# Kernel optimization log

Measured on AMD Instinct MI355X. Metric: run time of the kernel, lower is better.

## Reference

```python
import jax, jax.numpy as jnp
import numpy as np

B, T, F = 512, 512, 16
UNITS = [64, 32, 32, 32]
VOCAB, EDIM = 1281, 4


def setup_inputs() -> dict:
    key = jax.random.key(0)
    ks = jax.random.split(key, 32)
    x = jax.random.normal(ks[0], (B, T, F), jnp.float32)
    # column 1 holds integer org ids (stored as float, as in the TF model)
    ids = jax.random.randint(ks[1], (B, T), 0, VOCAB).astype(jnp.float32)
    x = x.at[:, :, 1].set(ids)
    d = {"input_tensor": x,
         "emb": jax.random.normal(ks[2], (VOCAB, EDIM), jnp.float32) * 0.05}
    din = 1 + (F - 2) + EDIM  # 18
    i = 3
    for l, u in enumerate(UNITS):
        d[f"k{l}"] = jax.random.normal(ks[i], (din, 3 * u), jnp.float32) * 0.1; i += 1
        d[f"r{l}"] = jax.random.normal(ks[i], (u, 3 * u), jnp.float32) * 0.1; i += 1
        d[f"bi{l}"] = jnp.zeros((3 * u,), jnp.float32)
        d[f"bh{l}"] = jnp.zeros((3 * u,), jnp.float32)
        din = u
    u = UNITS[-1]
    d["w1"] = jax.random.normal(ks[i], (u, u), jnp.float32) * 0.1; i += 1
    d["b1"] = jnp.zeros((u,), jnp.float32)
    d["w2"] = jax.random.normal(ks[i], (u, u), jnp.float32) * 0.1; i += 1
    d["b2"] = jnp.zeros((u,), jnp.float32)
    d["v"] = jax.random.normal(ks[i], (u, 1), jnp.float32) * 0.1; i += 1
    d["bv"] = jnp.zeros((1,), jnp.float32)
    d["wd"] = jax.random.normal(ks[i], (u, 2), jnp.float32) * 0.1; i += 1
    d["bd"] = jnp.zeros((2,), jnp.float32)
    return d


def _gru(h, xp, rk, bh):
    # Keras GRUCell (reset_after=True). xp = x @ kernel + input_bias, [B, 3u]
    hp = h @ rk + bh
    xz, xr, xh = jnp.split(xp, 3, axis=-1)
    hz, hr, hhp = jnp.split(hp, 3, axis=-1)
    z = jax.nn.sigmoid(xz + hz)
    r = jax.nn.sigmoid(xr + hr)
    hh = jnp.tanh(xh + r * hhp)
    return z * h + (1.0 - z) * hh


def _forward(input_tensor, emb, k0, r0, bi0, bh0, k1, r1, bi1, bh1,
             k2, r2, bi2, bh2, k3, r3, bi3, bh3,
             w1, b1, w2, b2, v, bv, wd, bd):
    f0 = input_tensor[:, :, :1]                      # [B,T,1]
    ids = input_tensor[:, :, 1].astype(jnp.int32)    # [B,T]
    rest = input_tensor[:, :, 2:]                    # [B,T,F-2]
    e = emb[ids]                                     # [B,T,4]
    inp = jnp.concatenate([f0, rest, e], axis=2)     # [B,T,din]

    # precompute layer-0 input projection as one big GEMM
    xp0 = inp @ k0 + bi0                             # [B,T,3*64]
    bsz = inp.shape[0]
    init = tuple(jnp.zeros((bsz, u), inp.dtype) for u in UNITS)

    def step(carry, xp_t):
        h0, h1, h2, h3 = carry
        h0 = _gru(h0, xp_t, r0, bh0)
        h1 = _gru(h1, h0 @ k1 + bi1, r1, bh1)
        h2 = _gru(h2, h1 @ k2 + bi2, r2, bh2)
        h3 = _gru(h3, h2 @ k3 + bi3, r3, bh3)
        return (h0, h1, h2, h3), h3

    (_, _, _, hT), seq = jax.lax.scan(step, init, jnp.swapaxes(xp0, 0, 1))
    outputs = jnp.swapaxes(seq, 0, 1)                # [B,T,32] (last-layer sequence)

    # Bahdanau attention: query = final state of last layer
    score = jnp.tanh(outputs @ w1 + b1 + (hT @ w2 + b2)[:, None, :]) @ v + bv  # [B,T,1]
    attn = jax.nn.softmax(score, axis=1)
    ctx = jnp.sum(attn * outputs, axis=1)            # [B,32]
    return jax.nn.softmax(ctx @ wd + bd, axis=-1)    # [B,2]


def reference(input_tensor, emb, k0, r0, bi0, bh0, k1, r1, bi1, bh1,
              k2, r2, bi2, bh2, k3, r3, bi3, bh3,
              w1, b1, w2, b2, v, bv, wd, bd):
    return _forward(input_tensor, emb, k0, r0, bi0, bh0, k1, r1, bi1, bh1,
                    k2, r2, bi2, bh2, k3, r3, bi3, bh3,
                    w1, b1, w2, b2, v, bv, wd, bd)
```

## Files before the change

### kernel.cpp

```cpp
#include <hip/hip_runtime.h>

#define TLEN 512
#define FIN 16

__device__ __forceinline__ float sigm(float x) { return 1.0f / (1.0f + __expf(-x)); }
__device__ __forceinline__ float tanh_f(float x) {
  x = fminf(fmaxf(x, -15.0f), 15.0f);
  float e = __expf(2.0f * x);
  return (e - 1.0f) / (e + 1.0f);
}

__device__ __forceinline__ float gru_fin(float own_main, float own_xh, float own_hhp,
                                         int role, float hold) {
  const float oth_main = __shfl_xor(own_main, 1);
  const float xh  = own_xh  + __shfl_xor(own_xh, 1);
  const float hhp = own_hhp + __shfl_xor(own_hhp, 1);
  const float sz = role ? oth_main : own_main;
  const float sr = role ? own_main : oth_main;
  const float z = sigm(sz);
  const float r = sigm(sr);
  const float hh = tanh_f(xh + r * hhp);
  return z * hold + (1.f - z) * hh;
}

__global__ __launch_bounds__(256, 1)
void rnn_pipe3(const float* __restrict__ x, const float* __restrict__ emb,
               const float* __restrict__ k0, const float* __restrict__ r0,
               const float* __restrict__ bi0, const float* __restrict__ bh0,
               const float* __restrict__ k1, const float* __restrict__ r1,
               const float* __restrict__ bi1, const float* __restrict__ bh1,
               const float* __restrict__ k2, const float* __restrict__ r2,
               const float* __restrict__ bi2, const float* __restrict__ bh2,
               const float* __restrict__ k3, const float* __restrict__ r3,
               const float* __restrict__ bi3, const float* __restrict__ bh3,
               const float* __restrict__ w1, const float* __restrict__ b1,
               const float* __restrict__ w2, const float* __restrict__ b2,
               const float* __restrict__ vv, const float* __restrict__ bv,
               const float* __restrict__ wd, const float* __restrict__ bd,
               float* __restrict__ out, float* __restrict__ obuf)
{
  __shared__ __align__(16) float s_xin[TLEN][20][2];
  __shared__ __align__(16) float s_h0[2][64][2];
  __shared__ __align__(16) float s_h1[2][32][2];
  __shared__ __align__(16) float s_h2[2][32][2];
  __shared__ __align__(16) float s_h3[2][32][2];
  __shared__ __align__(16) float s_pA[2][64][2];
  __shared__ __align__(16) float s_pAh[2][64][2];
  __shared__ __align__(16) float s_fl[2][16][2][32];
  __shared__ __align__(16) float e_w1[1024];
  __shared__ __align__(16) float e_sc[1024];
  __shared__ float e_hw2[64], e_b1[32], e_v[32], e_ctx[64];

  const int tid  = threadIdx.x;
  const int wid  = tid >> 6;
  const int lane = tid & 63;
  const int g    = lane >> 1;
  const int role = lane & 1;
  const int bb0  = blockIdx.x * 2;

  float Wa[96], Wb[48], Wc[48];
  float bm = 0.f, bxh = 0.f, bhh = 0.f;
  float cbm = 0.f, cbxh = 0.f, cbhh = 0.f;

  if (wid <= 1) {
    const int u  = wid * 32 + g;
    const int cm = role ? 64 + u : u;
    #pragma unroll
    for (int j = 0; j < 19; ++j) Wa[j] = k0[j*192 + cm];
    Wa[19] = 0.f;
    #pragma unroll
    for (int j = 0; j < 64; ++j) Wa[20+j] = r0[j*192 + cm];
    #pragma unroll
    for (int jj = 0; jj < 10; ++jj) {
      const int row = role*10 + jj;
      Wb[jj] = (row < 19) ? k0[row*192 + 128 + u] : 0.f;
    }
    #pragma unroll
    for (int jj = 0; jj < 32; ++jj) Wb[10+jj] = r0[(role*32+jj)*192 + 128 + u];
    bm  = bi0[cm] + bh0[cm];
    bxh = role ? 0.f : bi0[128+u];
    bhh = role ? bh0[128+u] : 0.f;
  }
  if (wid == 0) {
    const int cma = role ? 32 + g : g;
    #pragma unroll
    for (int j = 0; j < 32; ++j) Wc[j] = k3[j*96 + cma];
    #pragma unroll
    for (int jj = 0; jj < 16; ++jj) Wc[32+jj] = k3[(role*16+jj)*96 + 64 + g];
  }
  if (wid == 2) {
    const int cm = role ? 32 + g : g;
    #pragma unroll
    for (int j = 0; j < 64; ++j) Wa[j] = k1[j*96 + cm];
    #pragma unroll
    for (int j = 0; j < 32; ++j) Wa[64+j] = r1[j*96 + cm];
    #pragma unroll
    for (int jj = 0; jj < 32; ++jj) Wb[jj] = k1[(role*32+jj)*96 + 64 + g];
    #pragma unroll
    for (int jj = 0; jj < 16; ++jj) Wb[32+jj] = r1[(role*16+jj)*96 + 64 + g];
    bm  = bi1[cm] + bh1[cm];
    bxh = role ? 0.f : bi1[64+g];
    bhh = role ? bh1[64+g] : 0.f;
  }
  if (wid == 3) {
    const int cm = role ? 32 + g : g;
    #pragma unroll
    for (int j = 0; j < 32; ++j) Wa[j] = k2[j*96 + cm];
    #pragma unroll
    for (int j = 0; j < 32; ++j) Wa[32+j] = r2[j*96 + cm];
    #pragma unroll
    for (int jj = 0; jj < 16; ++jj) Wb[jj] = k2[(role*16+jj)*96 + 64 + g];
    #pragma unroll
    for (int jj = 0; jj < 16; ++jj) Wb[16+jj] = r2[(role*16+jj)*96 + 64 + g];
    bm  = bi2[cm] + bh2[cm];
    bxh = role ? 0.f : bi2[64+g];
    bhh = role ? bh2[64+g] : 0.f;
    #pragma unroll
    for (int j = 0; j < 32; ++j) Wc[j] = r3[j*96 + cm];
    #pragma unroll
    for (int jj = 0; jj < 16; ++jj) Wc[32+jj] = r3[(role*16+jj)*96 + 64 + g];
    cbm  = bi3[cm] + bh3[cm];
    cbxh = bi3[64+g];
    cbhh = bh3[64+g];
  }

  ((float*)s_h0)[tid] = 0.f;
  if (tid < 128) {
    ((float*)s_h1)[tid] = 0.f;
    ((float*)s_h2)[tid] = 0.f;
    ((float*)s_h3)[tid] = 0.f;
  }

  for (int r = tid; r < 2*TLEN; r += 256) {
    const int b2 = r & 1, t2 = r >> 1;
    const float* xr = &x[((size_t)(bb0+b2)*TLEN + t2)*FIN];
    const float4 x0 = *(const float4*)(xr);
    const float4 x1 = *(const float4*)(xr+4);
    const float4 x2 = *(const float4*)(xr+8);
    const float4 x3 = *(const float4*)(xr+12);
    float v[20];
    v[0]=x0.x; v[1]=x0.z; v[2]=x0.w;
    v[3]=x1.x; v[4]=x1.y; v[5]=x1.z; v[6]=x1.w;
    v[7]=x2.x; v[8]=x2.y; v[9]=x2.z; v[10]=x2.w;
    v[11]=x3.x; v[12]=x3.y; v[13]=x3.z; v[14]=x3.w;
    const int id = (int)x0.y;
    const float4 e4 = *(const float4*)&emb[id*4];
    v[15]=e4.x; v[16]=e4.y; v[17]=e4.z; v[18]=e4.w; v[19]=0.f;
    #pragma unroll
    for (int j = 0; j < 20; ++j) s_xin[t2][j][b2] = v[j];
  }

  auto flush = [&](int c) {
    const int par = c & 1;
    #pragma unroll
    for (int it = 0; it < 4; ++it) {
      const int f4 = it*64 + lane;
      const int u4 = f4 & 7, row = f4 >> 3;
      const int dt = row >> 1, b2 = row & 1;
      const float4 vq = *(const float4*)&s_fl[par][dt][b2][u4*4];
      *(float4*)&obuf[(((size_t)(bb0+b2)*TLEN) + c*16 + dt)*32 + u4*4] = vq;
    }
  };

  for (int i = 0; i < 516; ++i) {
    __syncthreads();
    const int wp = i & 1;
    const int rp = wp ^ 1;

    if (wid <= 1) {
      if (i < 512) {
        const int u = wid*32 + g;
        float a0A = bm, a0B = bm, a1A = 0.f, a1B = 0.f;
        #pragma unroll
        for (int j = 0; j < 20; j += 2) {
          const float4 q = *(const float4*)&s_xin[i][j][0];
          a0A += Wa[j]*q.x;   a0B += Wa[j]*q.y;
          a1A += Wa[j+1]*q.z; a1B += Wa[j+1]*q.w;
        }
        #pragma unroll
        for (int j = 0; j < 64; j += 2) {
          const float4 q = *(const float4*)&s_h0[rp][j][0];
          a0A += Wa[20+j]*q.x; a0B += Wa[20+j]*q.y;
          a1A += Wa[21+j]*q.z; a1B += Wa[21+j]*q.w;
        }
        float xqA = bxh, xqB = bxh;
        #pragma unroll
        for (int jj = 0; jj < 10; ++jj) {
          const float2 d = *(const float2*)&s_xin[i][role*10+jj][0];
          xqA += Wb[jj]*d.x; xqB += Wb[jj]*d.y;
        }
        float p0A = bhh, p0B = bhh, p1A = 0.f, p1B = 0.f;
        #pragma unroll
        for (int jj = 0; jj < 32; jj += 2) {
          const float4 q = *(const float4*)&s_h0[rp][role*32+jj][0];
          p0A += Wb[10+jj]*q.x; p0B += Wb[10+jj]*q.y;
          p1A += Wb[11+jj]*q.z; p1B += Wb[11+jj]*q.w;
        }
        const float holdA = s_h0[rp][u][0];
        const float holdB = s_h0[rp][u][1];
        const float hnA = gru_fin(a0A+a1A, xqA, p0A+p1A, role, holdA);
        const float hnB = gru_fin(a0B+a1B, xqB, p0B+p1B, role, holdB);
        if (!role) { s_h0[wp][u][0] = hnA; s_h0[wp][u][1] = hnB; }
      }
      if (wid == 0) {
        if (i >= 3 && i <= 514) {
          float q0A=0.f,q0B=0.f,q1A=0.f,q1B=0.f;
          #pragma unroll
          for (int j = 0; j < 32; j += 2) {
            const float4 q = *(const float4*)&s_h2[rp][j][0];
            q0A += Wc[j]*q.x;   q0B += Wc[j]*q.y;
            q1A += Wc[j+1]*q.z; q1B += Wc[j+1]*q.w;
          }
          float phA=0.f, phB=0.f, ph1A=0.f, ph1B=0.f;
          #pragma unroll
          for (int jj = 0; jj < 16; jj += 2) {
            const float4 q = *(const float4*)&s_h2[rp][role*16+jj][0];
            phA  += Wc[32+jj]*q.x; phB  += Wc[32+jj]*q.y;
            ph1A += Wc[33+jj]*q.z; ph1B += Wc[33+jj]*q.w;
          }
          s_pA[wp][lane][0]  = q0A+q1A;  s_pA[wp][lane][1]  = q0B+q1B;
          s_pAh[wp][lane][0] = phA+ph1A; s_pAh[wp][lane][1] = phB+ph1B;
        }
      } else {
        if (i >= 20 && ((i - 20) & 15) == 0) flush((i - 20) >> 4);
      }
    } else if (wid == 2) {
      if (i >= 1 && i <= 512) {
        float a0A = bm, a0B = bm, a1A=0.f, a1B=0.f;
        #pragma unroll
        for (int j = 0; j < 64; j += 2) {
          const float4 q = *(const float4*)&s_h0[rp][j][0];
          a0A += Wa[j]*q.x;   a0B += Wa[j]*q.y;
          a1A += Wa[j+1]*q.z; a1B += Wa[j+1]*q.w;
        }
        #pragma unroll
        for (int j = 0; j < 32; j += 2) {
          const float4 q = *(const float4*)&s_h1[rp][j][0];
          a0A += Wa[64+j]*q.x; a0B += Wa[64+j]*q.y;
          a1A += Wa[65+j]*q.z; a1B += Wa[65+j]*q.w;
        }
        float x0A = bxh, x0B = bxh, x1A = 0.f, x1B = 0.f;
        #pragma unroll
        for (int jj = 0; jj < 32; jj += 2) {
          const float4 q = *(const float4*)&s_h0[rp][role*32+jj][0];
          x0A += Wb[jj]*q.x;   x0B += Wb[jj]*q.y;
          x1A += Wb[jj+1]*q.z; x1B += Wb[jj+1]*q.w;
        }
        float p0A = bhh, p0B = bhh, p1A = 0.f, p1B = 0.f;
        #pragma unroll
        for (int jj = 0; jj < 16; jj += 2) {
          const float4 q = *(const float4*)&s_h1[rp][role*16+jj][0];
          p0A += Wb[32+jj]*q.x; p0B += Wb[32+jj]*q.y;
          p1A += Wb[33+jj]*q.z; p1B += Wb[33+jj]*q.w;
        }
        const float holdA = s_h1[rp][g][0];
        const float holdB = s_h1[rp][g][1];
        const float hnA = gru_fin(a0A+a1A, x0A+x1A, p0A+p1A, role, holdA);
        const float hnB = gru_fin(a0B+a1B, x0B+x1B, p0B+p1B, role, holdB);
        if (!role) { s_h1[wp][g][0] = hnA; s_h1[wp][g][1] = hnB; }
      }
    } else {
      if (i >= 2 && i <= 513) {
        float a0A = bm, a0B = bm, a1A=0.f, a1B=0.f;
        #pragma unroll
        for (int j = 0; j < 32; j += 2) {
          const float4 q = *(const float4*)&s_h1[rp][j][0];
          a0A += Wa[j]*q.x;   a0B += Wa[j]*q.y;
          a1A += Wa[j+1]*q.z; a1B += Wa[j+1]*q.w;
        }
        #pragma unroll
        for (int j = 0; j < 32; j += 2) {
          const float4 q = *(const float4*)&s_h2[rp][j][0];
          a0A += Wa[32+j]*q.x; a0B += Wa[32+j]*q.y;
          a1A += Wa[33+j]*q.z; a1B += Wa[33+j]*q.w;
        }
        float x0A = bxh, x0B = bxh, x1A = 0.f, x1B = 0.f;
        #pragma unroll
        for (int jj = 0; jj < 16; jj += 2) {
          const float4 q = *(const float4*)&s_h1[rp][role*16+jj][0];
          x0A += Wb[jj]*q.x;   x0B += Wb[jj]*q.y;
          x1A += Wb[jj+1]*q.z; x1B += Wb[jj+1]*q.w;
        }
        float p0A = bhh, p0B = bhh, p1A = 0.f, p1B = 0.f;
        #pragma unroll
        for (int jj = 0; jj < 16; jj += 2) {
          const float4 q = *(const float4*)&s_h2[rp][role*16+jj][0];
          p0A += Wb[16+jj]*q.x; p0B += Wb[16+jj]*q.y;
          p1A += Wb[17+jj]*q.z; p1B += Wb[17+jj]*q.w;
        }
        const float holdA = s_h2[rp][g][0];
        const float holdB = s_h2[rp][g][1];
        const float hnA = gru_fin(a0A+a1A, x0A+x1A, p0A+p1A, role, holdA);
        const float hnB = gru_fin(a0B+a1B, x0B+x1B, p0B+p1B, role, holdB);
        if (!role) { s_h2[wp][g][0] = hnA; s_h2[wp][g][1] = hnB; }
      }
      if (i >= 4) {
        float q0A=0.f,q0B=0.f,q1A=0.f,q1B=0.f;
        #pragma unroll
        for (int jj = 0; jj < 32; jj += 2) {
          const float4 q = *(const float4*)&s_h3[rp][jj][0];
          q0A += Wc[jj]*q.x;   q0B += Wc[jj]*q.y;
          q1A += Wc[jj+1]*q.z; q1B += Wc[jj+1]*q.w;
        }
        float ph0A=0.f, ph0B=0.f, ph1A=0.f, ph1B=0.f;
        #pragma unroll
        for (int jj = 0; jj < 16; jj += 2) {
          const float4 q = *(const float4*)&s_h3[rp][role*16+jj][0];
          ph0A += Wc[32+jj]*q.x; ph0B += Wc[32+jj]*q.y;
          ph1A += Wc[33+jj]*q.z; ph1B += Wc[33+jj]*q.w;
        }
        const float mainA = s_pA[rp][lane][0] + q0A + q1A + cbm;
        const float mainB = s_pA[rp][lane][1] + q0B + q1B + cbm;
        const float xhA_own = s_pAh[rp][lane][0];
        const float xhB_own = s_pAh[rp][lane][1];
        const float phA_own = ph0A + ph1A;
        const float phB_own = ph0B + ph1B;

        const float othA = __shfl_xor(mainA, 1);
        const float othB = __shfl_xor(mainB, 1);
        const float xhA = xhA_own + __shfl_xor(xhA_own, 1) + cbxh;
        const float xhB = xhB_own + __shfl_xor(xhB_own, 1) + cbxh;
        const float hhpA = phA_own + __shfl_xor(phA_own, 1) + cbhh;
        const float hhpB = phB_own + __shfl_xor(phB_own, 1) + cbhh;

        const float szA = role ? othA : mainA;
        const float srA = role ? mainA : othA;
        const float szB = role ? othB : mainB;
        const float srB = role ? mainB : othB;
        const float zA = sigm(szA), rA = sigm(srA);
        const float zB = sigm(szB), rB = sigm(srB);
        const float hhA = tanh_f(xhA + rA*hhpA);
        const float hhB = tanh_f(xhB + rB*hhpB);
        const float hnA = zA*s_h3[rp][g][0] + (1.f-zA)*hhA;
        const float hnB = zB*s_h3[rp][g][1] + (1.f-zB)*hhB;
        if (!role) {
          s_h3[wp][g][0] = hnA;
          s_h3[wp][g][1] = hnB;
          const int t3 = i - 4;
          s_fl[(t3>>4)&1][t3&15][0][g] = hnA;
          s_fl[(t3>>4)&1][t3&15][1][g] = hnB;
        }
      }
    }
  }
  __syncthreads();

  if (wid == 1) flush(31);

  for (int kk = tid; kk < 1024; kk += 256) e_w1[kk] = w1[kk];
  if (tid < 32) { e_b1[tid] = b1[tid]; e_v[tid] = vv[tid]; }
  if (tid >= 64 && tid < 128) {
    const int u = tid & 31, bb = (tid - 64) >> 5;
    float s = b2[u];
    #pragma unroll
    for (int j = 0; j < 32; ++j) s += s_h3[1][j][bb] * w2[j*32 + u];
    e_hw2[bb*32 + u] = s;
  }
  __syncthreads();

  #pragma unroll
  for (int c = 0; c < 4; ++c) {
    const int idx = c*256 + tid;
    const int bb = idx >> 9, t2 = idx & 511;
    const float* row = obuf + ((size_t)(bb0+bb)*TLEN + t2)*32;
    float rr[32];
    #pragma unroll
    for (int j = 0; j < 32; j += 4) {
      const float4 r4 = *(const float4*)&row[j];
      rr[j]=r4.x; rr[j+1]=r4.y; rr[j+2]=r4.z; rr[j+3]=r4.w;
    }
    float sc = 0.f;
    for (int u = 0; u < 32; ++u) {
      float qv = e_b1[u] + e_hw2[bb*32 + u];
      #pragma unroll
      for (int j = 0; j < 32; ++j) qv += rr[j]*e_w1[j*32+u];
      sc += tanh_f(qv)*e_v[u];
    }
    e_sc[idx] = sc;
  }
  __syncthreads();

  {
    if (wid < 2) {
      const int bb = wid;
      float sv[8]; float m = -1e30f;
      #pragma unroll
      for (int k = 0; k < 8; ++k) { sv[k] = e_sc[bb*512 + lane + 64*k]; m = fmaxf(m, sv[k]); }
      #pragma unroll
      for (int off = 32; off > 0; off >>= 1) m = fmaxf(m, __shfl_xor(m, off));
      float ss = 0.f;
      #pragma unroll
      for (int k = 0; k < 8; ++k) { sv[k] = __expf(sv[k]-m); ss += sv[k]; }
      #pragma unroll
      for (int off = 32; off > 0; off >>= 1) ss += __shfl_xor(ss, off);
      const float inv = 1.f/ss;
      #pragma unroll
      for (int k = 0; k < 8; ++k) e_sc[bb*512 + lane + 64*k] = sv[k]*inv;
    }
  }
  __syncthreads();

  if (tid < 64) {
    const int u = tid & 31, bb = tid >> 5;
    float acc = 0.f;
    const float* orow = obuf + (size_t)(bb0+bb)*TLEN*32 + u;
    const float* prow = e_sc + bb*512;
    #pragma unroll 4
    for (int t2 = 0; t2 < 512; ++t2) acc += prow[t2]*orow[(size_t)t2*32];
    e_ctx[bb*32 + u] = acc;
  }
  __syncthreads();

  if (tid < 2) {
    const int bb = tid;
    float l0 = bd[0], l1 = bd[1];
    #pragma unroll
    for (int u = 0; u < 32; ++u) {
      const float cv = e_ctx[bb*32 + u];
      l0 += cv*wd[u*2]; l1 += cv*wd[u*2+1];
    }
    const float mm = fmaxf(l0, l1);
    const float ex0 = __expf(l0-mm), ex1 = __expf(l1-mm);
    const float den = ex0 + ex1;
    out[(bb0+bb)*2 + 0] = ex0/den;
    out[(bb0+bb)*2 + 1] = ex1/den;
  }
}

extern "C" void kernel_launch(void* const* d_in, const int* in_sizes, int n_in,
                              void* d_out, int out_size, void* d_ws, size_t ws_size,
                              hipStream_t stream) {
  const float* x   = (const float*)d_in[0];
  const float* emb = (const float*)d_in[1];
  const float* k0  = (const float*)d_in[2];
  const float* r0  = (const float*)d_in[3];
  const float* bi0 = (const float*)d_in[4];
  const float* bh0 = (const float*)d_in[5];
  const float* k1  = (const float*)d_in[6];
  const float* r1  = (const float*)d_in[7];
  const float* bi1 = (const float*)d_in[8];
  const float* bh1 = (const float*)d_in[9];
  const float* k2  = (const float*)d_in[10];
  const float* r2  = (const float*)d_in[11];
  const float* bi2 = (const float*)d_in[12];
  const float* bh2 = (const float*)d_in[13];
  const float* k3  = (const float*)d_in[14];
  const float* r3  = (const float*)d_in[15];
  const float* bi3 = (const float*)d_in[16];
  const float* bh3 = (const float*)d_in[17];
  const float* w1  = (const float*)d_in[18];
  const float* b1  = (const float*)d_in[19];
  const float* w2  = (const float*)d_in[20];
  const float* b2  = (const float*)d_in[21];
  const float* v   = (const float*)d_in[22];
  const float* bv  = (const float*)d_in[23];
  const float* wd  = (const float*)d_in[24];
  const float* bd  = (const float*)d_in[25];

  float* out  = (float*)d_out;
  float* obuf = (float*)d_ws;

  rnn_pipe3<<<dim3(256), dim3(256), 0, stream>>>(
      x, emb, k0, r0, bi0, bh0, k1, r1, bi1, bh1,
      k2, r2, bi2, bh2, k3, r3, bi3, bh3,
      w1, b1, w2, b2, v, bv, wd, bd, out, obuf);
}
```

Baseline: 1.252 ms.

## Batch four timesteps per barrier in the GRU layer pipeline with ring-buffered states

The wavefront-per-layer pipeline now advances four timesteps between block barriers instead of one, cutting the barrier count from 516 to 133. Hidden states live in 8-slot ring buffers in shared memory. Each thread now owns one hidden unit for one batch element and computes all three gates itself, which removes the paired-lane shuffles. Layer 3's input projection is computed one superstep ahead on waves 0/1, and output flushing is spread across supersteps. In exchange, each wave runs a longer serial chain per superstep and holds many more weight registers, which adds register pressure and longer pipeline fill and drain.

```diff
diff --git a/kernel.cpp b/kernel.cpp
--- a/kernel.cpp
+++ b/kernel.cpp
@@ -10,43 +10,29 @@
   return (e - 1.0f) / (e + 1.0f);
 }
 
-__device__ __forceinline__ float gru_fin(float own_main, float own_xh, float own_hhp,
-                                         int role, float hold) {
-  const float oth_main = __shfl_xor(own_main, 1);
-  const float xh  = own_xh  + __shfl_xor(own_xh, 1);
-  const float hhp = own_hhp + __shfl_xor(own_hhp, 1);
-  const float sz = role ? oth_main : own_main;
-  const float sr = role ? own_main : oth_main;
-  const float z = sigm(sz);
-  const float r = sigm(sr);
-  const float hh = tanh_f(xh + r * hhp);
-  return z * hold + (1.f - z) * hh;
-}
-
 __global__ __launch_bounds__(256, 1)
-void rnn_pipe3(const float* __restrict__ x, const float* __restrict__ emb,
-               const float* __restrict__ k0, const float* __restrict__ r0,
-               const float* __restrict__ bi0, const float* __restrict__ bh0,
-               const float* __restrict__ k1, const float* __restrict__ r1,
-               const float* __restrict__ bi1, const float* __restrict__ bh1,
-               const float* __restrict__ k2, const float* __restrict__ r2,
-               const float* __restrict__ bi2, const float* __restrict__ bh2,
-               const float* __restrict__ k3, const float* __restrict__ r3,
-               const float* __restrict__ bi3, const float* __restrict__ bh3,
-               const float* __restrict__ w1, const float* __restrict__ b1,
-               const float* __restrict__ w2, const float* __restrict__ b2,
-               const float* __restrict__ vv, const float* __restrict__ bv,
-               const float* __restrict__ wd, const float* __restrict__ bd,
-               float* __restrict__ out, float* __restrict__ obuf)
+void rnn_k4(const float* __restrict__ x, const float* __restrict__ emb,
+            const float* __restrict__ k0, const float* __restrict__ r0,
+            const float* __restrict__ bi0, const float* __restrict__ bh0,
+            const float* __restrict__ k1, const float* __restrict__ r1,
+            const float* __restrict__ bi1, const float* __restrict__ bh1,
+            const float* __restrict__ k2, const float* __restrict__ r2,
+            const float* __restrict__ bi2, const float* __restrict__ bh2,
+            const float* __restrict__ k3, const float* __restrict__ r3,
+            const float* __restrict__ bi3, const float* __restrict__ bh3,
+            const float* __restrict__ w1, const float* __restrict__ b1,
+            const float* __restrict__ w2, const float* __restrict__ b2,
+            const float* __restrict__ vv, const float* __restrict__ bv,
+            const float* __restrict__ wd, const float* __restrict__ bd,
+            float* __restrict__ out, float* __restrict__ obuf)
 {
-  __shared__ __align__(16) float s_xin[TLEN][20][2];
-  __shared__ __align__(16) float s_h0[2][64][2];
-  __shared__ __align__(16) float s_h1[2][32][2];
-  __shared__ __align__(16) float s_h2[2][32][2];
-  __shared__ __align__(16) float s_h3[2][32][2];
-  __shared__ __align__(16) float s_pA[2][64][2];
-  __shared__ __align__(16) float s_pAh[2][64][2];
-  __shared__ __align__(16) float s_fl[2][16][2][32];
+  __shared__ __align__(16) float s_xin[2][TLEN][20];
+  __shared__ __align__(16) float s_h0[2][8][64];
+  __shared__ __align__(16) float s_h1[2][8][32];
+  __shared__ __align__(16) float s_h2[2][8][32];
+  __shared__ __align__(16) float s_h3[2][8][32];
+  __shared__ __align__(16) float s_pA[2][4][2][3][32];
+  __shared__ __align__(16) float s_fl[2][4][2][32];
   __shared__ __align__(16) float e_w1[1024];
   __shared__ __align__(16) float e_sc[1024];
   __shared__ float e_hw2[64], e_b1[32], e_v[32], e_ctx[64];
@@ -54,298 +40,241 @@
   const int tid  = threadIdx.x;
   const int wid  = tid >> 6;
   const int lane = tid & 63;
-  const int g    = lane >> 1;
-  const int role = lane & 1;
   const int bb0  = blockIdx.x * 2;
 
-  float Wa[96], Wb[48], Wc[48];
-  float bm = 0.f, bxh = 0.f, bhh = 0.f;
-  float cbm = 0.f, cbxh = 0.f, cbhh = 0.f;
+  float W1[192], W2[96], W3[96];
+  float bz=0.f, br=0.f, bxh=0.f, bhh=0.f;
+  float cz=0.f, cr=0.f, cxh=0.f, chh=0.f;
 
   if (wid <= 1) {
-    const int u  = wid * 32 + g;
-    const int cm = role ? 64 + u : u;
-    #pragma unroll
-    for (int j = 0; j < 19; ++j) Wa[j] = k0[j*192 + cm];
-    Wa[19] = 0.f;
-    #pragma unroll
-    for (int j = 0; j < 64; ++j) Wa[20+j] = r0[j*192 + cm];
-    #pragma unroll
-    for (int jj = 0; jj < 10; ++jj) {
-      const int row = role*10 + jj;
-      Wb[jj] = (row < 19) ? k0[row*192 + 128 + u] : 0.f;
-    }
-    #pragma unroll
-    for (int jj = 0; jj < 32; ++jj) Wb[10+jj] = r0[(role*32+jj)*192 + 128 + u];
-    bm  = bi0[cm] + bh0[cm];
-    bxh = role ? 0.f : bi0[128+u];
-    bhh = role ? bh0[128+u] : 0.f;
-  }
-  if (wid == 0) {
-    const int cma = role ? 32 + g : g;
-    #pragma unroll
-    for (int j = 0; j < 32; ++j) Wc[j] = k3[j*96 + cma];
-    #pragma unroll
-    for (int jj = 0; jj < 16; ++jj) Wc[32+jj] = k3[(role*16+jj)*96 + 64 + g];
-  }
-  if (wid == 2) {
-    const int cm = role ? 32 + g : g;
-    #pragma unroll
-    for (int j = 0; j < 64; ++j) Wa[j] = k1[j*96 + cm];
-    #pragma unroll
-    for (int j = 0; j < 32; ++j) Wa[64+j] = r1[j*96 + cm];
-    #pragma unroll
-    for (int jj = 0; jj < 32; ++jj) Wb[jj] = k1[(role*32+jj)*96 + 64 + g];
-    #pragma unroll
-    for (int jj = 0; jj < 16; ++jj) Wb[32+jj] = r1[(role*16+jj)*96 + 64 + g];
-    bm  = bi1[cm] + bh1[cm];
-    bxh = role ? 0.f : bi1[64+g];
-    bhh = role ? bh1[64+g] : 0.f;
-  }
-  if (wid == 3) {
-    const int cm = role ? 32 + g : g;
-    #pragma unroll
-    for (int j = 0; j < 32; ++j) Wa[j] = k2[j*96 + cm];
-    #pragma unroll
-    for (int j = 0; j < 32; ++j) Wa[32+j] = r2[j*96 + cm];
-    #pragma unroll
-    for (int jj = 0; jj < 16; ++jj) Wb[jj] = k2[(role*16+jj)*96 + 64 + g];
-    #pragma unroll
-    for (int jj = 0; jj < 16; ++jj) Wb[16+jj] = r2[(role*16+jj)*96 + 64 + g];
-    bm  = bi2[cm] + bh2[cm];
-    bxh = role ? 0.f : bi2[64+g];
-    bhh = role ? bh2[64+g] : 0.f;
-    #pragma unroll
-    for (int j = 0; j < 32; ++j) Wc[j] = r3[j*96 + cm];
-    #pragma unroll
-    for (int jj = 0; jj < 16; ++jj) Wc[32+jj] = r3[(role*16+jj)*96 + 64 + g];
-    cbm  = bi3[cm] + bh3[cm];
-    cbxh = bi3[64+g];
-    cbhh = bh3[64+g];
-  }
-
-  ((float*)s_h0)[tid] = 0.f;
-  if (tid < 128) {
-    ((float*)s_h1)[tid] = 0.f;
-    ((float*)s_h2)[tid] = 0.f;
-    ((float*)s_h3)[tid] = 0.f;
+    const int u = lane;
+    #pragma unroll
+    for (int g = 0; g < 3; ++g)
+      #pragma unroll
+      for (int j = 0; j < 64; ++j) W1[g*64+j] = r0[j*192 + g*64 + u];
+    #pragma unroll
+    for (int g = 0; g < 3; ++g)
+      #pragma unroll
+      for (int j = 0; j < 19; ++j) W2[g*19+j] = k0[j*192 + g*64 + u];
+    const int ku = lane & 31;
+    #pragma unroll
+    for (int g = 0; g < 3; ++g)
+      #pragma unroll
+      for (int j = 0; j < 32; ++j) W3[g*32+j] = k3[j*96 + g*32 + ku];
+    bz  = bi0[u]      + bh0[u];
+    br  = bi0[64+u]   + bh0[64+u];
+    bxh = bi0[128+u];
+    bhh = bh0[128+u];
+  } else if (wid == 2) {
+    const int u = lane & 31;
+    #pragma unroll
+    for (int g = 0; g < 3; ++g)
+      #pragma unroll
+      for (int j = 0; j < 64; ++j) W1[g*64+j] = k1[j*96 + g*32 + u];
+    #pragma unroll
+    for (int g = 0; g < 3; ++g)
+      #pragma unroll
+      for (int j = 0; j < 32; ++j) W2[g*32+j] = r1[j*96 + g*32 + u];
+    bz  = bi1[u]     + bh1[u];
+    br  = bi1[32+u]  + bh1[32+u];
+    bxh = bi1[64+u];
+    bhh = bh1[64+u];
+  } else {
+    const int u = lane & 31;
+    #pragma unroll
+    for (int g = 0; g < 3; ++g)
+      #pragma unroll
+      for (int j = 0; j < 32; ++j) W1[g*32+j] = k2[j*96 + g*32 + u];
+    #pragma unroll
+    for (int g = 0; g < 3; ++g)
+      #pragma unroll
+      for (int j = 0; j < 32; ++j) W1[96 + g*32+j] = r2[j*96 + g*32 + u];
+    #pragma unroll
+    for (int g = 0; g < 3; ++g)
+      #pragma unroll
+      for (int j = 0; j < 32; ++j) W2[g*32+j] = r3[j*96 + g*32 + u];
+    bz  = bi2[u]     + bh2[u];
+    br  = bi2[32+u]  + bh2[32+u];
+    bxh = bi2[64+u];
+    bhh = bh2[64+u];
+    cz  = bi3[u]     + bh3[u];
+    cr  = bi3[32+u]  + bh3[32+u];
+    cxh = bi3[64+u];
+    chh = bh3[64+u];
+  }
+
+  for (int q = tid; q < 1024; q += 256) ((float*)s_h0)[q] = 0.f;
+  for (int q = tid; q < 512; q += 256) {
+    ((float*)s_h1)[q] = 0.f; ((float*)s_h2)[q] = 0.f; ((float*)s_h3)[q] = 0.f;
   }
 
   for (int r = tid; r < 2*TLEN; r += 256) {
-    const int b2 = r & 1, t2 = r >> 1;
-    const float* xr = &x[((size_t)(bb0+b2)*TLEN + t2)*FIN];
+    const int b = r >> 9, t = r & 511;
+    const float* xr = &x[((size_t)(bb0 + b) * TLEN + t) * FIN];
     const float4 x0 = *(const float4*)(xr);
-    const float4 x1 = *(const float4*)(xr+4);
-    const float4 x2 = *(const float4*)(xr+8);
-    const float4 x3 = *(const float4*)(xr+12);
-    float v[20];
-    v[0]=x0.x; v[1]=x0.z; v[2]=x0.w;
-    v[3]=x1.x; v[4]=x1.y; v[5]=x1.z; v[6]=x1.w;
-    v[7]=x2.x; v[8]=x2.y; v[9]=x2.z; v[10]=x2.w;
-    v[11]=x3.x; v[12]=x3.y; v[13]=x3.z; v[14]=x3.w;
+    const float4 x1 = *(const float4*)(xr + 4);
+    const float4 x2 = *(const float4*)(xr + 8);
+    const float4 x3 = *(const float4*)(xr + 12);
     const int id = (int)x0.y;
-    const float4 e4 = *(const float4*)&emb[id*4];
-    v[15]=e4.x; v[16]=e4.y; v[17]=e4.z; v[18]=e4.w; v[19]=0.f;
-    #pragma unroll
-    for (int j = 0; j < 20; ++j) s_xin[t2][j][b2] = v[j];
-  }
-
-  auto flush = [&](int c) {
-    const int par = c & 1;
-    #pragma unroll
-    for (int it = 0; it < 4; ++it) {
-      const int f4 = it*64 + lane;
-      const int u4 = f4 & 7, row = f4 >> 3;
-      const int dt = row >> 1, b2 = row & 1;
-      const float4 vq = *(const float4*)&s_fl[par][dt][b2][u4*4];
-      *(float4*)&obuf[(((size_t)(bb0+b2)*TLEN) + c*16 + dt)*32 + u4*4] = vq;
-    }
-  };
-
-  for (int i = 0; i < 516; ++i) {
+    const float4 e4 = *(const float4*)&emb[id * 4];
+    float4* dst = (float4*)&s_xin[b][t][0];
+    dst[0] = make_float4(x0.x, x0.z, x0.w, x1.x);
+    dst[1] = make_float4(x1.y, x1.z, x1.w, x2.x);
+    dst[2] = make_float4(x2.y, x2.z, x2.w, x3.x);
+    dst[3] = make_float4(x3.y, x3.z, x3.w, e4.x);
+    dst[4] = make_float4(e4.y, e4.z, e4.w, 0.f);
+  }
+
+  float hold0 = 0.f, hold1 = 0.f, hold2 = 0.f, hold3 = 0.f;
+
+  for (int I = 0; I < 133; ++I) {
     __syncthreads();
-    const int wp = i & 1;
-    const int rp = wp ^ 1;
 
     if (wid <= 1) {
-      if (i < 512) {
-        const int u = wid*32 + g;
-        float a0A = bm, a0B = bm, a1A = 0.f, a1B = 0.f;
-        #pragma unroll
-        for (int j = 0; j < 20; j += 2) {
-          const float4 q = *(const float4*)&s_xin[i][j][0];
-          a0A += Wa[j]*q.x;   a0B += Wa[j]*q.y;
-          a1A += Wa[j+1]*q.z; a1B += Wa[j+1]*q.w;
-        }
-        #pragma unroll
-        for (int j = 0; j < 64; j += 2) {
-          const float4 q = *(const float4*)&s_h0[rp][j][0];
-          a0A += Wa[20+j]*q.x; a0B += Wa[20+j]*q.y;
-          a1A += Wa[21+j]*q.z; a1B += Wa[21+j]*q.w;
-        }
-        float xqA = bxh, xqB = bxh;
-        #pragma unroll
-        for (int jj = 0; jj < 10; ++jj) {
-          const float2 d = *(const float2*)&s_xin[i][role*10+jj][0];
-          xqA += Wb[jj]*d.x; xqB += Wb[jj]*d.y;
-        }
-        float p0A = bhh, p0B = bhh, p1A = 0.f, p1B = 0.f;
-        #pragma unroll
-        for (int jj = 0; jj < 32; jj += 2) {
-          const float4 q = *(const float4*)&s_h0[rp][role*32+jj][0];
-          p0A += Wb[10+jj]*q.x; p0B += Wb[10+jj]*q.y;
-          p1A += Wb[11+jj]*q.z; p1B += Wb[11+jj]*q.w;
-        }
-        const float holdA = s_h0[rp][u][0];
-        const float holdB = s_h0[rp][u][1];
-        const float hnA = gru_fin(a0A+a1A, xqA, p0A+p1A, role, holdA);
-        const float hnB = gru_fin(a0B+a1B, xqB, p0B+p1B, role, holdB);
-        if (!role) { s_h0[wp][u][0] = hnA; s_h0[wp][u][1] = hnB; }
-      }
-      if (wid == 0) {
-        if (i >= 3 && i <= 514) {
-          float q0A=0.f,q0B=0.f,q1A=0.f,q1B=0.f;
-          #pragma unroll
-          for (int j = 0; j < 32; j += 2) {
-            const float4 q = *(const float4*)&s_h2[rp][j][0];
-            q0A += Wc[j]*q.x;   q0B += Wc[j]*q.y;
-            q1A += Wc[j+1]*q.z; q1B += Wc[j+1]*q.w;
-          }
-          float phA=0.f, phB=0.f, ph1A=0.f, ph1B=0.f;
-          #pragma unroll
-          for (int jj = 0; jj < 16; jj += 2) {
-            const float4 q = *(const float4*)&s_h2[rp][role*16+jj][0];
-            phA  += Wc[32+jj]*q.x; phB  += Wc[32+jj]*q.y;
-            ph1A += Wc[33+jj]*q.z; ph1B += Wc[33+jj]*q.w;
-          }
-          s_pA[wp][lane][0]  = q0A+q1A;  s_pA[wp][lane][1]  = q0B+q1B;
-          s_pAh[wp][lane][0] = phA+ph1A; s_pAh[wp][lane][1] = phB+ph1B;
-        }
-      } else {
-        if (i >= 20 && ((i - 20) & 15) == 0) flush((i - 20) >> 4);
+      const int b = wid;
+      if (I >= 3 && I < 131) {
+        const int kb = lane >> 5, ku = lane & 31;
+        #pragma unroll
+        for (int s2 = 0; s2 < 2; ++s2) {
+          const int s = wid*2 + s2;
+          const int t = 4*(I-3) + s, sl = t & 7;
+          float pz = 0.f, pr = 0.f, ph = 0.f;
+          #pragma unroll
+          for (int j4 = 0; j4 < 8; ++j4) {
+            const float4 h4 = *(const float4*)&s_h2[kb][sl][j4*4];
+            pz += W3[j4*4]*h4.x + W3[j4*4+1]*h4.y + W3[j4*4+2]*h4.z + W3[j4*4+3]*h4.w;
+            pr += W3[32+j4*4]*h4.x + W3[32+j4*4+1]*h4.y + W3[32+j4*4+2]*h4.z + W3[32+j4*4+3]*h4.w;
+            ph += W3[64+j4*4]*h4.x + W3[64+j4*4+1]*h4.y + W3[64+j4*4+2]*h4.z + W3[64+j4*4+3]*h4.w;
+          }
+          const int pp = I & 1;
+          s_pA[pp][s][kb][0][ku] = pz;
+          s_pA[pp][s][kb][1][ku] = pr;
+          s_pA[pp][s][kb][2][ku] = ph;
+        }
+      }
+      if (wid == 1 && I >= 5) {
+        const int par = (I-1) & 1, t0 = 4*(I-5);
+        const int s = lane >> 4, fb = (lane >> 3) & 1, u0 = (lane & 7) * 4;
+        const float4 vq = *(const float4*)&s_fl[par][s][fb][u0];
+        *(float4*)&obuf[((size_t)(bb0+fb)*TLEN + t0 + s)*32 + u0] = vq;
+      }
+      if (I < 128) {
+        const int u = lane;
+        #pragma unroll
+        for (int s = 0; s < 4; ++s) {
+          const int t = 4*I + s;
+          const int ps = (t-1) & 7, ws = t & 7;
+          float az = bz, ar = br, ahx = bxh, ph = bhh;
+          float xa[20];
+          {
+            const float* xv = &s_xin[b][t][0];
+            *(float4*)&xa[0]  = *(const float4*)(xv);
+            *(float4*)&xa[4]  = *(const float4*)(xv+4);
+            *(float4*)&xa[8]  = *(const float4*)(xv+8);
+            *(float4*)&xa[12] = *(const float4*)(xv+12);
+            *(float4*)&xa[16] = *(const float4*)(xv+16);
+          }
+          #pragma unroll
+          for (int j = 0; j < 19; ++j) {
+            az += W2[j]*xa[j]; ar += W2[19+j]*xa[j]; ahx += W2[38+j]*xa[j];
+          }
+          #pragma unroll
+          for (int j4 = 0; j4 < 16; ++j4) {
+            const float4 h4 = *(const float4*)&s_h0[b][ps][j4*4];
+            az  += W1[j4*4]*h4.x + W1[j4*4+1]*h4.y + W1[j4*4+2]*h4.z + W1[j4*4+3]*h4.w;
+            ar  += W1[64+j4*4]*h4.x + W1[64+j4*4+1]*h4.y + W1[64+j4*4+2]*h4.z + W1[64+j4*4+3]*h4.w;
+            ph  += W1[128+j4*4]*h4.x + W1[128+j4*4+1]*h4.y + W1[128+j4*4+2]*h4.z + W1[128+j4*4+3]*h4.w;
+          }
+          const float z = sigm(az), r = sigm(ar);
+          const float hh = tanh_f(ahx + r*ph);
+          hold0 = z*hold0 + (1.f - z)*hh;
+          s_h0[b][ws][u] = hold0;
+        }
       }
     } else if (wid == 2) {
-      if (i >= 1 && i <= 512) {
-        float a0A = bm, a0B = bm, a1A=0.f, a1B=0.f;
-        #pragma unroll
-        for (int j = 0; j < 64; j += 2) {
-          const float4 q = *(const float4*)&s_h0[rp][j][0];
-          a0A += Wa[j]*q.x;   a0B += Wa[j]*q.y;
-          a1A += Wa[j+1]*q.z; a1B += Wa[j+1]*q.w;
-        }
-        #pragma unroll
-        for (int j = 0; j < 32; j += 2) {
-          const float4 q = *(const float4*)&s_h1[rp][j][0];
-          a0A += Wa[64+j]*q.x; a0B += Wa[64+j]*q.y;
-          a1A += Wa[65+j]*q.z; a1B += Wa[65+j]*q.w;
-        }
-        float x0A = bxh, x0B = bxh, x1A = 0.f, x1B = 0.f;
-        #pragma unroll
-        for (int jj = 0; jj < 32; jj += 2) {
-          const float4 q = *(const float4*)&s_h0[rp][role*32+jj][0];
-          x0A += Wb[jj]*q.x;   x0B += Wb[jj]*q.y;
-          x1A += Wb[jj+1]*q.z; x1B += Wb[jj+1]*q.w;
-        }
-        float p0A = bhh, p0B = bhh, p1A = 0.f, p1B = 0.f;
-        #pragma unroll
-        for (int jj = 0; jj < 16; jj += 2) {
-          const float4 q = *(const float4*)&s_h1[rp][role*16+jj][0];
-          p0A += Wb[32+jj]*q.x; p0B += Wb[32+jj]*q.y;
-          p1A += Wb[33+jj]*q.z; p1B += Wb[33+jj]*q.w;
-        }
-        const float holdA = s_h1[rp][g][0];
-        const float holdB = s_h1[rp][g][1];
-        const float hnA = gru_fin(a0A+a1A, x0A+x1A, p0A+p1A, role, holdA);
-        const float hnB = gru_fin(a0B+a1B, x0B+x1B, p0B+p1B, role, holdB);
-        if (!role) { s_h1[wp][g][0] = hnA; s_h1[wp][g][1] = hnB; }
+      if (I >= 1 && I < 129) {
+        const int b = lane >> 5, u = lane & 31;
+        #pragma unroll
+        for (int s = 0; s < 4; ++s) {
+          const int t = 4*(I-1) + s;
+          const int ps = (t-1) & 7, ws = t & 7;
+          float az = bz, ar = br, ahx = bxh, ph = bhh;
+          #pragma unroll
+          for (int j4 = 0; j4 < 16; ++j4) {
+            const float4 h4 = *(const float4*)&s_h0[b][ws][j4*4];
+            az  += W1[j4*4]*h4.x + W1[j4*4+1]*h4.y + W1[j4*4+2]*h4.z + W1[j4*4+3]*h4.w;
+            ar  += W1[64+j4*4]*h4.x + W1[64+j4*4+1]*h4.y + W1[64+j4*4+2]*h4.z + W1[64+j4*4+3]*h4.w;
+            ahx += W1[128+j4*4]*h4.x + W1[128+j4*4+1]*h4.y + W1[128+j4*4+2]*h4.z + W1[128+j4*4+3]*h4.w;
+          }
+          #pragma unroll
+          for (int j4 = 0; j4 < 8; ++j4) {
+            const float4 h4 = *(const float4*)&s_h1[b][ps][j4*4];
+            az += W2[j4*4]*h4.x + W2[j4*4+1]*h4.y + W2[j4*4+2]*h4.z + W2[j4*4+3]*h4.w;
+            ar += W2[32+j4*4]*h4.x + W2[32+j4*4+1]*h4.y + W2[32+j4*4+2]*h4.z + W2[32+j4*4+3]*h4.w;
+            ph += W2[64+j4*4]*h4.x + W2[64+j4*4+1]*h4.y + W2[64+j4*4+2]*h4.z + W2[64+j4*4+3]*h4.w;
+          }
+          const float z = sigm(az), r = sigm(ar);
+          const float hh = tanh_f(ahx + r*ph);
+          hold1 = z*hold1 + (1.f - z)*hh;
+          s_h1[b][ws][u] = hold1;
+        }
       }
     } else {
-      if (i >= 2 && i <= 513) {
-        float a0A = bm, a0B = bm, a1A=0.f, a1B=0.f;
-        #pragma unroll
-        for (int j = 0; j < 32; j += 2) {
-          const float4 q = *(const float4*)&s_h1[rp][j][0];
-          a0A += Wa[j]*q.x;   a0B += Wa[j]*q.y;
-          a1A += Wa[j+1]*q.z; a1B += Wa[j+1]*q.w;
-        }
-        #pragma unroll
-        for (int j = 0; j < 32; j += 2) {
-          const float4 q = *(const float4*)&s_h2[rp][j][0];
-          a0A += Wa[32+j]*q.x; a0B += Wa[32+j]*q.y;
-          a1A += Wa[33+j]*q.z; a1B += Wa[33+j]*q.w;
-        }
-        float x0A = bxh, x0B = bxh, x1A = 0.f, x1B = 0.f;
-        #pragma unroll
-        for (int jj = 0; jj < 16; jj += 2) {
-          const float4 q = *(const float4*)&s_h1[rp][role*16+jj][0];
-          x0A += Wb[jj]*q.x;   x0B += Wb[jj]*q.y;
-          x1A += Wb[jj+1]*q.z; x1B += Wb[jj+1]*q.w;
-        }
-        float p0A = bhh, p0B = bhh, p1A = 0.f, p1B = 0.f;
-        #pragma unroll
-        for (int jj = 0; jj < 16; jj += 2) {
-          const float4 q = *(const float4*)&s_h2[rp][role*16+jj][0];
-          p0A += Wb[16+jj]*q.x; p0B += Wb[16+jj]*q.y;
-          p1A += Wb[17+jj]*q.z; p1B += Wb[17+jj]*q.w;
-        }
-        const float holdA = s_h2[rp][g][0];
-        const float holdB = s_h2[rp][g][1];
-        const float hnA = gru_fin(a0A+a1A, x0A+x1A, p0A+p1A, role, holdA);
-        const float hnB = gru_fin(a0B+a1B, x0B+x1B, p0B+p1B, role, holdB);
-        if (!role) { s_h2[wp][g][0] = hnA; s_h2[wp][g][1] = hnB; }
-      }
-      if (i >= 4) {
-        float q0A=0.f,q0B=0.f,q1A=0.f,q1B=0.f;
-        #pragma unroll
-        for (int jj = 0; jj < 32; jj += 2) {
-          const float4 q = *(const float4*)&s_h3[rp][jj][0];
-          q0A += Wc[jj]*q.x;   q0B += Wc[jj]*q.y;
-          q1A += Wc[jj+1]*q.z; q1B += Wc[jj+1]*q.w;
-        }
-        float ph0A=0.f, ph0B=0.f, ph1A=0.f, ph1B=0.f;
-        #pragma unroll
-        for (int jj = 0; jj < 16; jj += 2) {
-          const float4 q = *(const float4*)&s_h3[rp][role*16+jj][0];
-          ph0A += Wc[32+jj]*q.x; ph0B += Wc[32+jj]*q.y;
-          ph1A += Wc[33+jj]*q.z; ph1B += Wc[33+jj]*q.w;
-        }
-        const float mainA = s_pA[rp][lane][0] + q0A + q1A + cbm;
-        const float mainB = s_pA[rp][lane][1] + q0B + q1B + cbm;
-        const float xhA_own = s_pAh[rp][lane][0];
-        const float xhB_own = s_pAh[rp][lane][1];
-        const float phA_own = ph0A + ph1A;
-        const float phB_own = ph0B + ph1B;
-
-        const float othA = __shfl_xor(mainA, 1);
-        const float othB = __shfl_xor(mainB, 1);
-        const float xhA = xhA_own + __shfl_xor(xhA_own, 1) + cbxh;
-        const float xhB = xhB_own + __shfl_xor(xhB_own, 1) + cbxh;
-        const float hhpA = phA_own + __shfl_xor(phA_own, 1) + cbhh;
-        const float hhpB = phB_own + __shfl_xor(phB_own, 1) + cbhh;
-
-        const float szA = role ? othA : mainA;
-        const float srA = role ? mainA : othA;
-        const float szB = role ? othB : mainB;
-        const float srB = role ? mainB : othB;
-        const float zA = sigm(szA), rA = sigm(srA);
-        const float zB = sigm(szB), rB = sigm(srB);
-        const float hhA = tanh_f(xhA + rA*hhpA);
-        const float hhB = tanh_f(xhB + rB*hhpB);
-        const float hnA = zA*s_h3[rp][g][0] + (1.f-zA)*hhA;
-        const float hnB = zB*s_h3[rp][g][1] + (1.f-zB)*hhB;
-        if (!role) {
-          s_h3[wp][g][0] = hnA;
-          s_h3[wp][g][1] = hnB;
-          const int t3 = i - 4;
-          s_fl[(t3>>4)&1][t3&15][0][g] = hnA;
-          s_fl[(t3>>4)&1][t3&15][1][g] = hnB;
-        }
-      }
-    }
-  }
-  __syncthreads();
-
-  if (wid == 1) flush(31);
+      const int b = lane >> 5, u = lane & 31;
+      if (I >= 2 && I < 130) {
+        #pragma unroll
+        for (int s = 0; s < 4; ++s) {
+          const int t = 4*(I-2) + s;
+          const int ps = (t-1) & 7, ws = t & 7;
+          float az = bz, ar = br, ahx = bxh, ph = bhh;
+          #pragma unroll
+          for (int j4 = 0; j4 < 8; ++j4) {
+            const float4 h4 = *(const float4*)&s_h1[b][ws][j4*4];
+            az  += W1[j4*4]*h4.x + W1[j4*4+1]*h4.y + W1[j4*4+2]*h4.z + W1[j4*4+3]*h4.w;
+            ar  += W1[32+j4*4]*h4.x + W1[32+j4*4+1]*h4.y + W1[32+j4*4+2]*h4.z + W1[32+j4*4+3]*h4.w;
+            ahx += W1[64+j4*4]*h4.x + W1[64+j4*4+1]*h4.y + W1[64+j4*4+2]*h4.z + W1[64+j4*4+3]*h4.w;
+          }
+          #pragma unroll
+          for (int j4 = 0; j4 < 8; ++j4) {
+            const float4 h4 = *(const float4*)&s_h2[b][ps][j4*4];
+            az += W1[96+j4*4]*h4.x + W1[96+j4*4+1]*h4.y + W1[96+j4*4+2]*h4.z + W1[96+j4*4+3]*h4.w;
+            ar += W1[128+j4*4]*h4.x + W1[128+j4*4+1]*h4.y + W1[128+j4*4+2]*h4.z + W1[128+j4*4+3]*h4.w;
+            ph += W1[160+j4*4]*h4.x + W1[160+j4*4+1]*h4.y + W1[160+j4*4+2]*h4.z + W1[160+j4*4+3]*h4.w;
+          }
+          const float z = sigm(az), r = sigm(ar);
+          const float hh = tanh_f(ahx + r*ph);
+          hold2 = z*hold2 + (1.f - z)*hh;
+          s_h2[b][ws][u] = hold2;
+        }
+      }
+      if (I >= 4 && I < 132) {
+        #pragma unroll
+        for (int s = 0; s < 4; ++s) {
+          const int t = 4*(I-4) + s;
+          const int ps = (t-1) & 7, ws = t & 7;
+          float sz = 0.f, sr = 0.f, sh = 0.f;
+          #pragma unroll
+          for (int j4 = 0; j4 < 8; ++j4) {
+            const float4 h4 = *(const float4*)&s_h3[b][ps][j4*4];
+            sz += W2[j4*4]*h4.x + W2[j4*4+1]*h4.y + W2[j4*4+2]*h4.z + W2[j4*4+3]*h4.w;
+            sr += W2[32+j4*4]*h4.x + W2[32+j4*4+1]*h4.y + W2[32+j4*4+2]*h4.z + W2[32+j4*4+3]*h4.w;
+            sh += W2[64+j4*4]*h4.x + W2[64+j4*4+1]*h4.y + W2[64+j4*4+2]*h4.z + W2[64+j4*4+3]*h4.w;
+          }
+          const int pp = (I-1) & 1;
+          const float pz  = s_pA[pp][s][b][0][u];
+          const float pr  = s_pA[pp][s][b][1][u];
+          const float phh = s_pA[pp][s][b][2][u];
+          const float z = sigm(pz + sz + cz);
+          const float r = sigm(pr + sr + cr);
+          const float hh = tanh_f((phh + cxh) + r*(sh + chh));
+          hold3 = z*hold3 + (1.f - z)*hh;
+          s_h3[b][ws][u] = hold3;
+          s_fl[I & 1][s][b][u] = hold3;
+        }
+      }
+    }
+  }
+  __syncthreads();
 
   for (int kk = tid; kk < 1024; kk += 256) e_w1[kk] = w1[kk];
   if (tid < 32) { e_b1[tid] = b1[tid]; e_v[tid] = vv[tid]; }
@@ -353,7 +282,7 @@
     const int u = tid & 31, bb = (tid - 64) >> 5;
     float s = b2[u];
     #pragma unroll
-    for (int j = 0; j < 32; ++j) s += s_h3[1][j][bb] * w2[j*32 + u];
+    for (int j = 0; j < 32; ++j) s += s_h3[bb][7][j] * w2[j*32 + u];
     e_hw2[bb*32 + u] = s;
   }
   __syncthreads();
@@ -460,7 +389,7 @@
   float* out  = (float*)d_out;
   float* obuf = (float*)d_ws;
 
-  rnn_pipe3<<<dim3(256), dim3(256), 0, stream>>>(
+  rnn_k4<<<dim3(256), dim3(256), 0, stream>>>(
       x, emb, k0, r0, bi0, bh0, k1, r1, bi1, bh1,
       k2, r2, bi2, bh2, k3, r3, bi3, bh3,
       w1, b1, w2, b2, v, bv, wd, bd, out, obuf);
```

After: 4.616 ms. +268.8%, slower.
